# Kernel optimization log

Measured on AMD Instinct MI355X. Metric: run time of the kernel, lower is better.

## Reference

```python
import jax, jax.numpy as jnp
import numpy as np

HEADS = 8
DIM_HEAD = 64
SCALE = DIM_HEAD ** -0.5
QUERY_DIM = 512
CTX_DIM = 64
INNER = HEADS * DIM_HEAD  # 512
GATE_HID = 32


def setup_inputs() -> dict:
    key = jax.random.key(0)
    ks = jax.random.split(key, 11)
    B, N, M = 4, 2048, 2048
    s = lambda fan: 1.0 / np.sqrt(fan)
    return {
        "x": jax.random.normal(ks[0], (B, N, QUERY_DIM), dtype=jnp.float32),
        "context": jax.random.normal(ks[1], (B, M, CTX_DIM), dtype=jnp.float32),
        "Wq": jax.random.normal(ks[2], (QUERY_DIM, INNER), dtype=jnp.float32) * s(QUERY_DIM),
        "Wk": jax.random.normal(ks[3], (CTX_DIM, INNER), dtype=jnp.float32) * s(CTX_DIM),
        "Wv": jax.random.normal(ks[4], (CTX_DIM, INNER), dtype=jnp.float32) * s(CTX_DIM),
        "W1": jax.random.normal(ks[5], (CTX_DIM, GATE_HID), dtype=jnp.float32) * s(CTX_DIM),
        "b1": jnp.zeros((GATE_HID,), dtype=jnp.float32),
        "W2": jax.random.normal(ks[6], (GATE_HID, 1), dtype=jnp.float32) * s(GATE_HID),
        "b2": jnp.zeros((1,), dtype=jnp.float32),
        "Wo": jax.random.normal(ks[7], (INNER, QUERY_DIM), dtype=jnp.float32) * s(INNER),
        "bo": jnp.zeros((QUERY_DIM,), dtype=jnp.float32),
    }


def reference(x, context, Wq, Wk, Wv, W1, b1, W2, b2, Wo, bo):
    B, N, _ = x.shape
    M = context.shape[1]
    # visual reliability gate: sigmoid(relu(ctx @ W1 + b1) @ W2 + b2) -> [B, M, 1]
    gate = jax.nn.sigmoid(jax.nn.relu(context @ W1 + b1) @ W2 + b2)
    ctx = context * gate
    # projections
    q = (x @ Wq).reshape(B, N, HEADS, DIM_HEAD).transpose(0, 2, 1, 3)    # [B,H,N,D]
    k = (ctx @ Wk).reshape(B, M, HEADS, DIM_HEAD).transpose(0, 2, 1, 3)  # [B,H,M,D]
    v = (ctx @ Wv).reshape(B, M, HEADS, DIM_HEAD).transpose(0, 2, 1, 3)  # [B,H,M,D]
    # scaled dot-product attention (full score matrix, as in source)
    sim = jnp.einsum('bhid,bhjd->bhij', q, k) * SCALE
    attn = jax.nn.softmax(sim, axis=-1)
    out = jnp.einsum('bhij,bhjd->bhid', attn, v)
    out = out.transpose(0, 2, 1, 3).reshape(B, N, INNER)
    return out @ Wo + bo
```

## Files before the change

kernel.cpp:

```cpp
#include <hip/hip_runtime.h>

typedef unsigned short u16;
typedef unsigned int u32;
using frag16 = __attribute__((ext_vector_type(8))) short;
using facc   = __attribute__((ext_vector_type(4))) float;
using facc16 = __attribute__((ext_vector_type(16))) float;

#define DEV static __device__ __forceinline__

DEV u16 f2bf(float f) {
  union { float f; unsigned u; } v; v.f = f;
  unsigned r = v.u + 0x7fffu + ((v.u >> 16) & 1u);
  return (u16)(r >> 16);
}
DEV unsigned fbits(float f) {
  union { float f; unsigned u; } v; v.f = f;
  return v.u;
}
DEV unsigned pkbf(float lo, float hi) {
  return __builtin_amdgcn_perm(fbits(hi) + 0x8000u, fbits(lo) + 0x8000u, 0x07060302u);
}
DEV unsigned pkbf_t(float lo, float hi) {
  return __builtin_amdgcn_perm(fbits(hi), fbits(lo), 0x07060302u);
}
DEV void gld16(const u16* g, u16* l) {
  __builtin_amdgcn_global_load_lds(
      (__attribute__((address_space(1))) unsigned int*)(g),
      (__attribute__((address_space(3))) unsigned int*)(l), 16, 0, 0);
}

__global__ __launch_bounds__(256) void prep_gate_kernel(const float4* __restrict__ x,
    const float* __restrict__ Wq, const float* __restrict__ Wk,
    const float* __restrict__ Wv, const float* __restrict__ Wo,
    const float* __restrict__ ctx, const float* __restrict__ W1,
    const float* __restrict__ b1, const float* __restrict__ W2,
    const float* __restrict__ b2,
    u16* __restrict__ xb, u16* __restrict__ WqT, u16* __restrict__ WkT,
    u16* __restrict__ WvT, u16* __restrict__ WoT, u16* __restrict__ gctx) {
  int bid = blockIdx.x;
  if (bid < 4096) {
    int id = bid * 256 + threadIdx.x;
    float4 v = x[id];
    ushort4 o;
    o.x = f2bf(v.x); o.y = f2bf(v.y); o.z = f2bf(v.z); o.w = f2bf(v.w);
    *(ushort4*)(xb + (size_t)id * 4) = o;
  } else if (bid < 4240) {
    int job = bid - 4096;
    const float* W; u16* WT; int K, tile;
    if (job < 64)      { W = Wq; WT = WqT; K = 512; tile = job; }
    else if (job < 72) { W = Wk; WT = WkT; K = 64;  tile = job - 64; }
    else if (job < 80) { W = Wv; WT = WvT; K = 64;  tile = job - 72; }
    else               { W = Wo; WT = WoT; K = 512; tile = job - 80; }
    int tilesK = K >> 6;
    int tr = tile % tilesK, tc = tile / tilesK;
    __shared__ float tl[64][65];
    int c = threadIdx.x & 63, r4 = threadIdx.x >> 6;
    #pragma unroll
    for (int it = 0; it < 16; ++it) {
      int kk = it * 4 + r4;
      tl[kk][c] = W[(size_t)(tr * 64 + kk) * 512 + tc * 64 + c];
    }
    __syncthreads();
    #pragma unroll
    for (int it = 0; it < 16; ++it) {
      int nn = it * 4 + r4;
      WT[(size_t)(tc * 64 + nn) * K + tr * 64 + c] = f2bf(tl[c][nn]);
    }
  } else {
    int wave = threadIdx.x >> 6, lane = threadIdx.x & 63;
    int row = (bid - 4240) * 4 + wave;
    __shared__ float sc[4][64];
    float cv = ctx[(size_t)row * 64 + lane];
    sc[wave][lane] = cv;
    __syncthreads();
    float h = 0.f;
    if (lane < 32) {
      h = b1[lane];
      #pragma unroll
      for (int i = 0; i < 64; ++i) h += sc[wave][i] * W1[i * 32 + lane];
      h = fmaxf(h, 0.f) * W2[lane];
    }
    #pragma unroll
    for (int off = 32; off; off >>= 1) h += __shfl_xor(h, off);
    float g = 1.f / (1.f + __expf(-(h + b2[0])));
    gctx[(size_t)row * 64 + lane] = f2bf(cv * g);
  }
}

template<int MODE>
DEV void gemm128_body(const u16* __restrict__ A, const u16* __restrict__ BT,
                      void* __restrict__ Cp, const float* __restrict__ bias,
                      int m0, int n0, float scale,
                      u16* As0, u16* As1, u16* Bs0, u16* Bs1) {
  const int K = 512, N = 512;
  const int lane = threadIdx.x & 63, wave = threadIdx.x >> 6;
  const int quad = lane >> 4, l16 = lane & 15;
  const int wr = wave >> 1, wc = wave & 1;

  const u16* gA = A + (size_t)(m0 + wave * 32 + (lane >> 2)) * K + (lane & 3) * 8;
  const u16* gB = BT + (size_t)(n0 + wave * 16 + (lane >> 2)) * K + (lane & 3) * 8;

  facc acc[4][2] = {};

  for (int k0 = 0; k0 < K; k0 += 64) {
    if (k0) __syncthreads();
    gld16(gA + k0,           As0 + wave * 1024);
    gld16(gA + 16 * K + k0,  As0 + wave * 1024 + 512);
    gld16(gA + k0 + 32,          As1 + wave * 1024);
    gld16(gA + 16 * K + k0 + 32, As1 + wave * 1024 + 512);
    gld16(gB + k0,      Bs0 + wave * 512);
    gld16(gB + k0 + 32, Bs1 + wave * 512);
    __syncthreads();

    #pragma unroll
    for (int hh = 0; hh < 2; ++hh) {
      const u16* Ah = hh ? As1 : As0;
      const u16* Bh = hh ? Bs1 : Bs0;
      frag16 af[4], bf[2];
      #pragma unroll
      for (int rt = 0; rt < 4; ++rt)
        af[rt] = *(const frag16*)(Ah + (wr * 64 + rt * 16 + l16) * 32 + quad * 8);
      #pragma unroll
      for (int ct = 0; ct < 2; ++ct)
        bf[ct] = *(const frag16*)(Bh + (wc * 32 + ct * 16 + l16) * 32 + quad * 8);
      #pragma unroll
      for (int rt = 0; rt < 4; ++rt)
        #pragma unroll
        for (int ct = 0; ct < 2; ++ct)
          acc[rt][ct] = __builtin_amdgcn_mfma_f32_16x16x32_bf16(af[rt], bf[ct], acc[rt][ct], 0, 0, 0);
    }
  }

  #pragma unroll
  for (int rt = 0; rt < 4; ++rt) {
    #pragma unroll
    for (int ct = 0; ct < 2; ++ct) {
      int col = n0 + wc * 32 + ct * 16 + l16;
      int r0g = m0 + wr * 64 + rt * 16 + quad * 4;
      if (MODE == 0) {
        u16* C = (u16*)Cp;
        #pragma unroll
        for (int r = 0; r < 4; ++r)
          C[(size_t)(r0g + r) * N + col] = f2bf(acc[rt][ct][r] * scale);
      } else {
        float* C = (float*)Cp;
        float bv = bias[col];
        #pragma unroll
        for (int r = 0; r < 4; ++r)
          C[(size_t)(r0g + r) * N + col] = acc[rt][ct][r] + bv;
      }
    }
  }
}

__global__ __launch_bounds__(256) void proj_kernel(const u16* __restrict__ xb,
    const u16* __restrict__ WqT, u16* __restrict__ qb,
    const u16* __restrict__ gctx, const u16* __restrict__ BkT,
    const u16* __restrict__ BvT, u16* __restrict__ Kp, u16* __restrict__ Vp) {
  __shared__ __align__(16) u16 As0[128 * 32], As1[128 * 32];
  __shared__ __align__(16) u16 Bs0[64 * 32], Bs1[64 * 32];
  int bid = blockIdx.x;
  if (bid < 512) {
    int n0 = (bid & 7) * 64, m0 = (bid >> 3) * 128;
    gemm128_body<0>(xb, WqT, qb, nullptr, m0, n0,
                    0.125f * 1.4426950408889634f, As0, As1, Bs0, Bs1);
    return;
  }
  bid -= 512;
  const int Kd = 64;
  int lane = threadIdx.x & 63, wave = threadIdx.x >> 6;
  int quad = lane >> 4, l16 = lane & 15;
  int wr = wave >> 1, wc = wave & 1;
  int rowBase = (bid >> 3) * 64 + wr * 32;
  int colBase = (bid & 7) * 64 + wc * 32;
  facc ak[2][2] = {}, av[2][2] = {};
  const u16* a0 = gctx + (size_t)(rowBase + l16) * Kd + quad * 8;
  const u16* a1 = a0 + (size_t)16 * Kd;
  const u16* bk0 = BkT + (size_t)(colBase + l16) * Kd + quad * 8;
  const u16* bk1 = bk0 + (size_t)16 * Kd;
  const u16* bv0 = BvT + (size_t)(colBase + l16) * Kd + quad * 8;
  const u16* bv1 = bv0 + (size_t)16 * Kd;
  #pragma unroll
  for (int kk = 0; kk < Kd; kk += 32) {
    frag16 af0 = *(const frag16*)(a0 + kk);
    frag16 af1 = *(const frag16*)(a1 + kk);
    frag16 k0 = *(const frag16*)(bk0 + kk);
    frag16 k1 = *(const frag16*)(bk1 + kk);
    frag16 v0 = *(const frag16*)(bv0 + kk);
    frag16 v1 = *(const frag16*)(bv1 + kk);
    ak[0][0] = __builtin_amdgcn_mfma_f32_16x16x32_bf16(af0, k0, ak[0][0], 0, 0, 0);
    ak[0][1] = __builtin_amdgcn_mfma_f32_16x16x32_bf16(af0, k1, ak[0][1], 0, 0, 0);
    ak[1][0] = __builtin_amdgcn_mfma_f32_16x16x32_bf16(af1, k0, ak[1][0], 0, 0, 0);
    ak[1][1] = __builtin_amdgcn_mfma_f32_16x16x32_bf16(af1, k1, ak[1][1], 0, 0, 0);
    av[0][0] = __builtin_amdgcn_mfma_f32_16x16x32_bf16(af0, v0, av[0][0], 0, 0, 0);
    av[0][1] = __builtin_amdgcn_mfma_f32_16x16x32_bf16(af0, v1, av[0][1], 0, 0, 0);
    av[1][0] = __builtin_amdgcn_mfma_f32_16x16x32_bf16(af1, v0, av[1][0], 0, 0, 0);
    av[1][1] = __builtin_amdgcn_mfma_f32_16x16x32_bf16(af1, v1, av[1][1], 0, 0, 0);
  }
  #pragma unroll
  for (int rt = 0; rt < 2; ++rt) {
    #pragma unroll
    for (int ct = 0; ct < 2; ++ct) {
      int col = colBase + ct * 16 + l16;
      int r0g = rowBase + rt * 16 + quad * 4;
      int hh = col >> 6, d = col & 63;
      int b = r0g >> 11;
      #pragma unroll
      for (int r = 0; r < 4; ++r) {
        int m = (r0g + r) & 2047;
        size_t addr = ((((size_t)(b * 8 + hh) * 64 + (m >> 5)) * 4 + (d >> 4)) * 64
                       + ((d >> 3) & 1) * 32 + (m & 31)) * 8 + (d & 7);
        Kp[addr] = f2bf(ak[rt][ct][r]);
      }
      int m = r0g & 2047;
      size_t addr = ((((size_t)(b * 8 + hh) * 64 + (m >> 5)) * 4
                      + ((m >> 4) & 1) * 2 + (d >> 5)) * 64
                     + ((m >> 3) & 1) * 32 + (d & 31)) * 8 + (m & 7);
      ushort4 o;
      o.x = f2bf(av[rt][ct][0]); o.y = f2bf(av[rt][ct][1]);
      o.z = f2bf(av[rt][ct][2]); o.w = f2bf(av[rt][ct][3]);
      *(ushort4*)(Vp + addr) = o;
    }
  }
}

__global__ __launch_bounds__(256, 2) void attn_kernel(
    const u16* __restrict__ qb, const u16* __restrict__ Kp,
    const u16* __restrict__ Vp, u16* __restrict__ ob) {
  const int lane = threadIdx.x & 63, wave = threadIdx.x >> 6;
  const int l32 = lane & 31;
  const int hi = lane >> 5;
  const int bid = blockIdx.x;
  const int bh = bid & 31;
  const int qblk = bid >> 5;
  const int b = bh >> 3, h = bh & 7;
  const int q0 = (qblk * 4 + wave) * 32;
  const int rowg = b * 2048 + q0 + l32;

  __shared__ __align__(16) u16 sK[2][2][2048], sV[2][2][2048];

  const u16* qp = qb + (size_t)rowg * 512 + h * 64 + hi * 8;
  frag16 qf0 = *(const frag16*)(qp);
  frag16 qf1 = *(const frag16*)(qp + 16);
  frag16 qf2 = *(const frag16*)(qp + 32);
  frag16 qf3 = *(const frag16*)(qp + 48);

  frag16 ones;
  #pragma unroll
  for (int i = 0; i < 8; ++i) ones[i] = (short)0x3F80;

  facc16 O0 = {}, O1 = {}, Lacc = {};

  const size_t ts = 2048;
  const u16* kpb = Kp + (size_t)(bh * 64) * ts + wave * 512 + lane * 8;
  const u16* vpb = Vp + (size_t)(bh * 64) * ts + wave * 512 + lane * 8;

  gld16(kpb,      sK[0][0] + wave * 512);
  gld16(kpb + ts, sK[0][1] + wave * 512);
  gld16(vpb,      sV[0][0] + wave * 512);
  gld16(vpb + ts, sV[0][1] + wave * 512);

  for (int g = 0; g < 32; ++g) {
    const int p = g & 1;
    __syncthreads();
    if (g + 1 < 32) {
      const size_t t2 = (size_t)(2 * g + 2) * ts;
      gld16(kpb + t2,      sK[p ^ 1][0] + wave * 512);
      gld16(kpb + t2 + ts, sK[p ^ 1][1] + wave * 512);
      gld16(vpb + t2,      sV[p ^ 1][0] + wave * 512);
      gld16(vpb + t2 + ts, sV[p ^ 1][1] + wave * 512);
    }

    frag16 kfa[4], kfb[4];
    #pragma unroll
    for (int i = 0; i < 4; ++i) {
      kfa[i] = *(const frag16*)(sK[p][0] + i * 512 + lane * 8);
      kfb[i] = *(const frag16*)(sK[p][1] + i * 512 + lane * 8);
    }

    facc16 Sa = {}, Sb = {};
    Sa = __builtin_amdgcn_mfma_f32_32x32x16_bf16(kfa[0], qf0, Sa, 0, 0, 0);
    Sb = __builtin_amdgcn_mfma_f32_32x32x16_bf16(kfb[0], qf0, Sb, 0, 0, 0);
    Sa = __builtin_amdgcn_mfma_f32_32x32x16_bf16(kfa[1], qf1, Sa, 0, 0, 0);
    Sb = __builtin_amdgcn_mfma_f32_32x32x16_bf16(kfb[1], qf1, Sb, 0, 0, 0);
    Sa = __builtin_amdgcn_mfma_f32_32x32x16_bf16(kfa[2], qf2, Sa, 0, 0, 0);
    Sb = __builtin_amdgcn_mfma_f32_32x32x16_bf16(kfb[2], qf2, Sb, 0, 0, 0);
    Sa = __builtin_amdgcn_mfma_f32_32x32x16_bf16(kfa[3], qf3, Sa, 0, 0, 0);
    Sb = __builtin_amdgcn_mfma_f32_32x32x16_bf16(kfb[3], qf3, Sb, 0, 0, 0);

    float ea[16], eb[16];
    #pragma unroll
    for (int r = 0; r < 16; ++r) { ea[r] = __builtin_amdgcn_exp2f(Sa[r]);
                                   eb[r] = __builtin_amdgcn_exp2f(Sb[r]); }

    unsigned pua[2][4], pub[2][4];
    #pragma unroll
    for (int c = 0; c < 2; ++c) {
      {
        const float* ee = ea + c * 8;
        unsigned L0 = pkbf_t(ee[0], ee[1]);
        unsigned L1 = pkbf_t(ee[2], ee[3]);
        unsigned H0 = pkbf_t(ee[4], ee[5]);
        unsigned H1 = pkbf_t(ee[6], ee[7]);
        unsigned Y0 = hi ? L0 : H0;
        unsigned Y1 = hi ? L1 : H1;
        unsigned X0 = (unsigned)__shfl_xor((int)Y0, 32);
        unsigned X1 = (unsigned)__shfl_xor((int)Y1, 32);
        pua[c][0] = hi ? X0 : L0;
        pua[c][1] = hi ? X1 : L1;
        pua[c][2] = hi ? H0 : X0;
        pua[c][3] = hi ? H1 : X1;
      }
      {
        const float* ee = eb + c * 8;
        unsigned L0 = pkbf_t(ee[0], ee[1]);
        unsigned L1 = pkbf_t(ee[2], ee[3]);
        unsigned H0 = pkbf_t(ee[4], ee[5]);
        unsigned H1 = pkbf_t(ee[6], ee[7]);
        unsigned Y0 = hi ? L0 : H0;
        unsigned Y1 = hi ? L1 : H1;
        unsigned X0 = (unsigned)__shfl_xor((int)Y0, 32);
        unsigned X1 = (unsigned)__shfl_xor((int)Y1, 32);
        pub[c][0] = hi ? X0 : L0;
        pub[c][1] = hi ? X1 : L1;
        pub[c][2] = hi ? H0 : X0;
        pub[c][3] = hi ? H1 : X1;
      }
    }
    frag16 Pa0 = *(frag16*)&pua[0][0];
    frag16 Pa1 = *(frag16*)&pua[1][0];
    frag16 Pb0 = *(frag16*)&pub[0][0];
    frag16 Pb1 = *(frag16*)&pub[1][0];

    Lacc = __builtin_amdgcn_mfma_f32_32x32x16_bf16(ones, Pa0, Lacc, 0, 0, 0);
    Lacc = __builtin_amdgcn_mfma_f32_32x32x16_bf16(ones, Pa1, Lacc, 0, 0, 0);
    Lacc = __builtin_amdgcn_mfma_f32_32x32x16_bf16(ones, Pb0, Lacc, 0, 0, 0);
    Lacc = __builtin_amdgcn_mfma_f32_32x32x16_bf16(ones, Pb1, Lacc, 0, 0, 0);

    frag16 vfa[4], vfb[4];
    #pragma unroll
    for (int i = 0; i < 4; ++i) {
      vfa[i] = *(const frag16*)(sV[p][0] + i * 512 + lane * 8);
      vfb[i] = *(const frag16*)(sV[p][1] + i * 512 + lane * 8);
    }

    O0 = __builtin_amdgcn_mfma_f32_32x32x16_bf16(vfa[0], Pa0, O0, 0, 0, 0);
    O1 = __builtin_amdgcn_mfma_f32_32x32x16_bf16(vfa[1], Pa0, O1, 0, 0, 0);
    O0 = __builtin_amdgcn_mfma_f32_32x32x16_bf16(vfa[2], Pa1, O0, 0, 0, 0);
    O1 = __builtin_amdgcn_mfma_f32_32x32x16_bf16(vfa[3], Pa1, O1, 0, 0, 0);
    O0 = __builtin_amdgcn_mfma_f32_32x32x16_bf16(vfb[0], Pb0, O0, 0, 0, 0);
    O1 = __builtin_amdgcn_mfma_f32_32x32x16_bf16(vfb[1], Pb0, O1, 0, 0, 0);
    O0 = __builtin_amdgcn_mfma_f32_32x32x16_bf16(vfb[2], Pb1, O0, 0, 0, 0);
    O1 = __builtin_amdgcn_mfma_f32_32x32x16_bf16(vfb[3], Pb1, O1, 0, 0, 0);
  }

  float rinv = 1.0f / Lacc[0];

  u16* op = ob + (size_t)rowg * 512 + h * 64;
  #pragma unroll
  for (int dt = 0; dt < 2; ++dt) {
    #pragma unroll
    for (int rq = 0; rq < 4; ++rq) {
      float v0, v1, v2, v3;
      if (dt == 0) { v0 = O0[rq*4]; v1 = O0[rq*4+1]; v2 = O0[rq*4+2]; v3 = O0[rq*4+3]; }
      else         { v0 = O1[rq*4]; v1 = O1[rq*4+1]; v2 = O1[rq*4+2]; v3 = O1[rq*4+3]; }
      uint2 pk;
      pk.x = pkbf(v0 * rinv, v1 * rinv);
      pk.y = pkbf(v2 * rinv, v3 * rinv);
      int d0 = dt * 32 + 8 * rq + 4 * hi;
      *(uint2*)(op + d0) = pk;
    }
  }
}

__global__ __launch_bounds__(256) void gemm_out(const u16* __restrict__ A,
    const u16* __restrict__ BT, float* __restrict__ C,
    const float* __restrict__ bias) {
  __shared__ __align__(16) u16 As0[128 * 32], As1[128 * 32];
  __shared__ __align__(16) u16 Bs0[64 * 32], Bs1[64 * 32];
  int n0 = (blockIdx.x & 7) * 64, m0 = (blockIdx.x >> 3) * 128;
  gemm128_body<2>(A, BT, C, bias, m0, n0, 1.f, As0, As1, Bs0, Bs1);
}

extern "C" void kernel_launch(void* const* d_in, const int* in_sizes, int n_in,
                              void* d_out, int out_size, void* d_ws, size_t ws_size,
                              hipStream_t stream) {
  const float* x   = (const float*)d_in[0];
  const float* ctx = (const float*)d_in[1];
  const float* Wq  = (const float*)d_in[2];
  const float* Wk  = (const float*)d_in[3];
  const float* Wv  = (const float*)d_in[4];
  const float* W1  = (const float*)d_in[5];
  const float* b1  = (const float*)d_in[6];
  const float* W2  = (const float*)d_in[7];
  const float* b2  = (const float*)d_in[8];
  const float* Wo  = (const float*)d_in[9];
  const float* bo  = (const float*)d_in[10];
  float* out = (float*)d_out;

  char* ws = (char*)d_ws;
  size_t off = 0;
  auto alloc = [&](size_t bytes) {
    char* p = ws + off;
    off += (bytes + 255) & ~(size_t)255;
    return p;
  };
  u16* xb    = (u16*)alloc(8192ull * 512 * 2);
  u16* qb    = (u16*)alloc(8192ull * 512 * 2);
  u16* Kp    = (u16*)alloc(8192ull * 512 * 2);
  u16* Vp    = (u16*)alloc(8192ull * 512 * 2);
  u16* ob    = (u16*)alloc(8192ull * 512 * 2);
  u16* gctx  = (u16*)alloc(8192ull * 64 * 2);
  u16* WqT   = (u16*)alloc(512ull * 512 * 2);
  u16* WkT   = (u16*)alloc(512ull * 64 * 2);
  u16* WvT   = (u16*)alloc(512ull * 64 * 2);
  u16* WoT   = (u16*)alloc(512ull * 512 * 2);

  prep_gate_kernel<<<6288, 256, 0, stream>>>((const float4*)x, Wq, Wk, Wv, Wo,
                                             ctx, W1, b1, W2, b2,
                                             xb, WqT, WkT, WvT, WoT, gctx);
  proj_kernel<<<1536, 256, 0, stream>>>(xb, WqT, qb, gctx, WkT, WvT, Kp, Vp);
  attn_kernel<<<512, 256, 0, stream>>>(qb, Kp, Vp, ob);
  gemm_out<<<512, 256, 0, stream>>>(ob, WoT, out, bo);
}
```

Measured before the change: 166.9 us.

## Software-pipeline attention loop: overlap QK of next tile with softmax/PV of current

Restructures the attention main loop into a two-stage software pipeline: the QK^T MFMAs for the next K/V tile are issued before the exp/pack/PV work of the current tile, with explicit double-buffer staging and fewer barriers per pair of tiles. It also interleaves the row-sum MFMAs with the PV MFMAs and raises wave priority around MFMA bursts via s_setprio. The aim is to hide exp and shuffle latency behind matrix work, at the cost of more live accumulator registers, which may reduce occupancy.

```diff
diff --git a/kernel.cpp b/kernel.cpp
--- a/kernel.cpp
+++ b/kernel.cpp
@@ -250,48 +250,55 @@
   for (int i = 0; i < 8; ++i) ones[i] = (short)0x3F80;
 
   facc16 O0 = {}, O1 = {}, Lacc = {};
+  facc16 SA0, SA1, SB0, SB1;
 
   const size_t ts = 2048;
   const u16* kpb = Kp + (size_t)(bh * 64) * ts + wave * 512 + lane * 8;
   const u16* vpb = Vp + (size_t)(bh * 64) * ts + wave * 512 + lane * 8;
 
-  gld16(kpb,      sK[0][0] + wave * 512);
-  gld16(kpb + ts, sK[0][1] + wave * 512);
-  gld16(vpb,      sV[0][0] + wave * 512);
-  gld16(vpb + ts, sV[0][1] + wave * 512);
-
-  for (int g = 0; g < 32; ++g) {
-    const int p = g & 1;
-    __syncthreads();
-    if (g + 1 < 32) {
-      const size_t t2 = (size_t)(2 * g + 2) * ts;
-      gld16(kpb + t2,      sK[p ^ 1][0] + wave * 512);
-      gld16(kpb + t2 + ts, sK[p ^ 1][1] + wave * 512);
-      gld16(vpb + t2,      sV[p ^ 1][0] + wave * 512);
-      gld16(vpb + t2 + ts, sV[p ^ 1][1] + wave * 512);
-    }
-
+  u16* k0 = &sK[0][0][0]; u16* v0 = &sV[0][0][0];
+  u16* k1 = &sK[1][0][0]; u16* v1 = &sV[1][0][0];
+
+  auto STAGE = [&](int g, u16* dK, u16* dV) {
+    const size_t t2 = (size_t)(2 * g) * ts;
+    gld16(kpb + t2,      dK + wave * 512);
+    gld16(kpb + t2 + ts, dK + 2048 + wave * 512);
+    gld16(vpb + t2,      dV + wave * 512);
+    gld16(vpb + t2 + ts, dV + 2048 + wave * 512);
+  };
+
+  auto QK = [&](const u16* bK, facc16& S0, facc16& S1) {
     frag16 kfa[4], kfb[4];
     #pragma unroll
     for (int i = 0; i < 4; ++i) {
-      kfa[i] = *(const frag16*)(sK[p][0] + i * 512 + lane * 8);
-      kfb[i] = *(const frag16*)(sK[p][1] + i * 512 + lane * 8);
-    }
-
-    facc16 Sa = {}, Sb = {};
-    Sa = __builtin_amdgcn_mfma_f32_32x32x16_bf16(kfa[0], qf0, Sa, 0, 0, 0);
-    Sb = __builtin_amdgcn_mfma_f32_32x32x16_bf16(kfb[0], qf0, Sb, 0, 0, 0);
-    Sa = __builtin_amdgcn_mfma_f32_32x32x16_bf16(kfa[1], qf1, Sa, 0, 0, 0);
-    Sb = __builtin_amdgcn_mfma_f32_32x32x16_bf16(kfb[1], qf1, Sb, 0, 0, 0);
-    Sa = __builtin_amdgcn_mfma_f32_32x32x16_bf16(kfa[2], qf2, Sa, 0, 0, 0);
-    Sb = __builtin_amdgcn_mfma_f32_32x32x16_bf16(kfb[2], qf2, Sb, 0, 0, 0);
-    Sa = __builtin_amdgcn_mfma_f32_32x32x16_bf16(kfa[3], qf3, Sa, 0, 0, 0);
-    Sb = __builtin_amdgcn_mfma_f32_32x32x16_bf16(kfb[3], qf3, Sb, 0, 0, 0);
-
+      kfa[i] = *(const frag16*)(bK + i * 512 + lane * 8);
+      kfb[i] = *(const frag16*)(bK + 2048 + i * 512 + lane * 8);
+    }
+    facc16 sa = {}, sb = {};
+    __builtin_amdgcn_s_setprio(1);
+    sa = __builtin_amdgcn_mfma_f32_32x32x16_bf16(kfa[0], qf0, sa, 0, 0, 0);
+    sb = __builtin_amdgcn_mfma_f32_32x32x16_bf16(kfb[0], qf0, sb, 0, 0, 0);
+    sa = __builtin_amdgcn_mfma_f32_32x32x16_bf16(kfa[1], qf1, sa, 0, 0, 0);
+    sb = __builtin_amdgcn_mfma_f32_32x32x16_bf16(kfb[1], qf1, sb, 0, 0, 0);
+    sa = __builtin_amdgcn_mfma_f32_32x32x16_bf16(kfa[2], qf2, sa, 0, 0, 0);
+    sb = __builtin_amdgcn_mfma_f32_32x32x16_bf16(kfb[2], qf2, sb, 0, 0, 0);
+    sa = __builtin_amdgcn_mfma_f32_32x32x16_bf16(kfa[3], qf3, sa, 0, 0, 0);
+    sb = __builtin_amdgcn_mfma_f32_32x32x16_bf16(kfb[3], qf3, sb, 0, 0, 0);
+    __builtin_amdgcn_s_setprio(0);
+    S0 = sa; S1 = sb;
+  };
+
+  auto EPPV = [&](const facc16& S0, const facc16& S1, const u16* bV) {
+    frag16 vfa[4], vfb[4];
+    #pragma unroll
+    for (int i = 0; i < 4; ++i) {
+      vfa[i] = *(const frag16*)(bV + i * 512 + lane * 8);
+      vfb[i] = *(const frag16*)(bV + 2048 + i * 512 + lane * 8);
+    }
     float ea[16], eb[16];
     #pragma unroll
-    for (int r = 0; r < 16; ++r) { ea[r] = __builtin_amdgcn_exp2f(Sa[r]);
-                                   eb[r] = __builtin_amdgcn_exp2f(Sb[r]); }
+    for (int r = 0; r < 16; ++r) { ea[r] = __builtin_amdgcn_exp2f(S0[r]);
+                                   eb[r] = __builtin_amdgcn_exp2f(S1[r]); }
 
     unsigned pua[2][4], pub[2][4];
     #pragma unroll
@@ -332,27 +339,43 @@
     frag16 Pb0 = *(frag16*)&pub[0][0];
     frag16 Pb1 = *(frag16*)&pub[1][0];
 
+    __builtin_amdgcn_s_setprio(1);
     Lacc = __builtin_amdgcn_mfma_f32_32x32x16_bf16(ones, Pa0, Lacc, 0, 0, 0);
-    Lacc = __builtin_amdgcn_mfma_f32_32x32x16_bf16(ones, Pa1, Lacc, 0, 0, 0);
-    Lacc = __builtin_amdgcn_mfma_f32_32x32x16_bf16(ones, Pb0, Lacc, 0, 0, 0);
-    Lacc = __builtin_amdgcn_mfma_f32_32x32x16_bf16(ones, Pb1, Lacc, 0, 0, 0);
-
-    frag16 vfa[4], vfb[4];
-    #pragma unroll
-    for (int i = 0; i < 4; ++i) {
-      vfa[i] = *(const frag16*)(sV[p][0] + i * 512 + lane * 8);
-      vfb[i] = *(const frag16*)(sV[p][1] + i * 512 + lane * 8);
-    }
-
     O0 = __builtin_amdgcn_mfma_f32_32x32x16_bf16(vfa[0], Pa0, O0, 0, 0, 0);
     O1 = __builtin_amdgcn_mfma_f32_32x32x16_bf16(vfa[1], Pa0, O1, 0, 0, 0);
+    Lacc = __builtin_amdgcn_mfma_f32_32x32x16_bf16(ones, Pa1, Lacc, 0, 0, 0);
     O0 = __builtin_amdgcn_mfma_f32_32x32x16_bf16(vfa[2], Pa1, O0, 0, 0, 0);
     O1 = __builtin_amdgcn_mfma_f32_32x32x16_bf16(vfa[3], Pa1, O1, 0, 0, 0);
+    Lacc = __builtin_amdgcn_mfma_f32_32x32x16_bf16(ones, Pb0, Lacc, 0, 0, 0);
     O0 = __builtin_amdgcn_mfma_f32_32x32x16_bf16(vfb[0], Pb0, O0, 0, 0, 0);
     O1 = __builtin_amdgcn_mfma_f32_32x32x16_bf16(vfb[1], Pb0, O1, 0, 0, 0);
+    Lacc = __builtin_amdgcn_mfma_f32_32x32x16_bf16(ones, Pb1, Lacc, 0, 0, 0);
     O0 = __builtin_amdgcn_mfma_f32_32x32x16_bf16(vfb[2], Pb1, O0, 0, 0, 0);
     O1 = __builtin_amdgcn_mfma_f32_32x32x16_bf16(vfb[3], Pb1, O1, 0, 0, 0);
-  }
+    __builtin_amdgcn_s_setprio(0);
+  };
+
+  STAGE(0, k0, v0);
+  __syncthreads();
+  STAGE(1, k1, v1);
+  QK(k0, SA0, SA1);
+
+  #pragma unroll 1
+  for (int gg = 0; gg < 15; ++gg) {
+    const int g = 2 * gg;
+    EPPV(SA0, SA1, v0);
+    __syncthreads();
+    STAGE(g + 2, k0, v0);
+    QK(k1, SB0, SB1);
+    EPPV(SB0, SB1, v1);
+    __syncthreads();
+    STAGE(g + 3, k1, v1);
+    QK(k0, SA0, SA1);
+  }
+  EPPV(SA0, SA1, v0);
+  __syncthreads();
+  QK(k1, SB0, SB1);
+  EPPV(SB0, SB1, v1);
 
   float rinv = 1.0f / Lacc[0];
 
@@ -361,12 +384,12 @@
   for (int dt = 0; dt < 2; ++dt) {
     #pragma unroll
     for (int rq = 0; rq < 4; ++rq) {
-      float v0, v1, v2, v3;
-      if (dt == 0) { v0 = O0[rq*4]; v1 = O0[rq*4+1]; v2 = O0[rq*4+2]; v3 = O0[rq*4+3]; }
-      else         { v0 = O1[rq*4]; v1 = O1[rq*4+1]; v2 = O1[rq*4+2]; v3 = O1[rq*4+3]; }
+      float v0e, v1e, v2e, v3e;
+      if (dt == 0) { v0e = O0[rq*4]; v1e = O0[rq*4+1]; v2e = O0[rq*4+2]; v3e = O0[rq*4+3]; }
+      else         { v0e = O1[rq*4]; v1e = O1[rq*4+1]; v2e = O1[rq*4+2]; v3e = O1[rq*4+3]; }
       uint2 pk;
-      pk.x = pkbf(v0 * rinv, v1 * rinv);
-      pk.y = pkbf(v2 * rinv, v3 * rinv);
+      pk.x = pkbf(v0e * rinv, v1e * rinv);
+      pk.y = pkbf(v2e * rinv, v3e * rinv);
       int d0 = dt * 32 + 8 * rq + 4 * hi;
       *(uint2*)(op + d0) = pk;
     }
```

Result: no change. 169.0 us (+1.3%).

## Triple-buffer K/V tiles in attention with explicit vmcnt waits

Applied to the files above, without the earlier changes.

Moves the attention kernel's K/V shared-memory staging from double to triple buffering, prefetching two tiles ahead. Each iteration waits only on the older tile's loads via explicit s_waitcnt vmcnt and a raw barrier, and the next prefetch is issued after the K fragments are read, so it can be a single barrier per iteration. Shared memory rises from 32KB to 48KB per block, which may affect the two-blocks-per-CU occupancy, and correctness now depends on the hand-counted vmcnt value matching the number of outstanding loads.

```diff
diff --git a/kernel.cpp b/kernel.cpp
--- a/kernel.cpp
+++ b/kernel.cpp
@@ -237,7 +237,7 @@
   const int q0 = (qblk * 4 + wave) * 32;
   const int rowg = b * 2048 + q0 + l32;
 
-  __shared__ __align__(16) u16 sK[2][2][2048], sV[2][2][2048];
+  __shared__ __align__(16) u16 sK[3][2][2048], sV[3][2][2048];
 
   const u16* qp = qb + (size_t)rowg * 512 + h * 64 + hi * 8;
   frag16 qf0 = *(const frag16*)(qp);
@@ -255,27 +255,40 @@
   const u16* kpb = Kp + (size_t)(bh * 64) * ts + wave * 512 + lane * 8;
   const u16* vpb = Vp + (size_t)(bh * 64) * ts + wave * 512 + lane * 8;
 
-  gld16(kpb,      sK[0][0] + wave * 512);
-  gld16(kpb + ts, sK[0][1] + wave * 512);
-  gld16(vpb,      sV[0][0] + wave * 512);
-  gld16(vpb + ts, sV[0][1] + wave * 512);
-
+  auto STAGE = [&](int g, int buf) {
+    const size_t t2 = (size_t)(2 * g) * ts;
+    gld16(kpb + t2,      &sK[buf][0][0] + wave * 512);
+    gld16(kpb + t2 + ts, &sK[buf][1][0] + wave * 512);
+    gld16(vpb + t2,      &sV[buf][0][0] + wave * 512);
+    gld16(vpb + t2 + ts, &sV[buf][1][0] + wave * 512);
+  };
+
+  STAGE(0, 0);
+  STAGE(1, 1);
+
+  int p = 0;
+  #pragma unroll 1
   for (int g = 0; g < 32; ++g) {
-    const int p = g & 1;
-    __syncthreads();
-    if (g + 1 < 32) {
-      const size_t t2 = (size_t)(2 * g + 2) * ts;
-      gld16(kpb + t2,      sK[p ^ 1][0] + wave * 512);
-      gld16(kpb + t2 + ts, sK[p ^ 1][1] + wave * 512);
-      gld16(vpb + t2,      sV[p ^ 1][0] + wave * 512);
-      gld16(vpb + t2 + ts, sV[p ^ 1][1] + wave * 512);
-    }
+    if (g < 31) {
+      asm volatile("s_waitcnt vmcnt(4) lgkmcnt(0)" ::: "memory");
+    } else {
+      asm volatile("s_waitcnt vmcnt(0) lgkmcnt(0)" ::: "memory");
+    }
+    __builtin_amdgcn_s_barrier();
+
+    const u16* kbase = &sK[p][0][0];
+    const u16* vbase = &sV[p][0][0];
 
     frag16 kfa[4], kfb[4];
     #pragma unroll
     for (int i = 0; i < 4; ++i) {
-      kfa[i] = *(const frag16*)(sK[p][0] + i * 512 + lane * 8);
-      kfb[i] = *(const frag16*)(sK[p][1] + i * 512 + lane * 8);
+      kfa[i] = *(const frag16*)(kbase + i * 512 + lane * 8);
+      kfb[i] = *(const frag16*)(kbase + 2048 + i * 512 + lane * 8);
+    }
+
+    if (g + 2 < 32) {
+      int ps = p + 2; if (ps >= 3) ps -= 3;
+      STAGE(g + 2, ps);
     }
 
     facc16 Sa = {}, Sb = {};
@@ -340,8 +353,8 @@
     frag16 vfa[4], vfb[4];
     #pragma unroll
     for (int i = 0; i < 4; ++i) {
-      vfa[i] = *(const frag16*)(sV[p][0] + i * 512 + lane * 8);
-      vfb[i] = *(const frag16*)(sV[p][1] + i * 512 + lane * 8);
+      vfa[i] = *(const frag16*)(vbase + i * 512 + lane * 8);
+      vfb[i] = *(const frag16*)(vbase + 2048 + i * 512 + lane * 8);
     }
 
     O0 = __builtin_amdgcn_mfma_f32_32x32x16_bf16(vfa[0], Pa0, O0, 0, 0, 0);
@@ -352,6 +365,8 @@
     O1 = __builtin_amdgcn_mfma_f32_32x32x16_bf16(vfb[1], Pb0, O1, 0, 0, 0);
     O0 = __builtin_amdgcn_mfma_f32_32x32x16_bf16(vfb[2], Pb1, O0, 0, 0, 0);
     O1 = __builtin_amdgcn_mfma_f32_32x32x16_bf16(vfb[3], Pb1, O1, 0, 0, 0);
+
+    ++p; if (p == 3) p = 0;
   }
 
   float rinv = 1.0f / Lacc[0];
@@ -361,12 +376,12 @@
   for (int dt = 0; dt < 2; ++dt) {
     #pragma unroll
     for (int rq = 0; rq < 4; ++rq) {
-      float v0, v1, v2, v3;
-      if (dt == 0) { v0 = O0[rq*4]; v1 = O0[rq*4+1]; v2 = O0[rq*4+2]; v3 = O0[rq*4+3]; }
-      else         { v0 = O1[rq*4]; v1 = O1[rq*4+1]; v2 = O1[rq*4+2]; v3 = O1[rq*4+3]; }
+      float v0e, v1e, v2e, v3e;
+      if (dt == 0) { v0e = O0[rq*4]; v1e = O0[rq*4+1]; v2e = O0[rq*4+2]; v3e = O0[rq*4+3]; }
+      else         { v0e = O1[rq*4]; v1e = O1[rq*4+1]; v2e = O1[rq*4+2]; v3e = O1[rq*4+3]; }
       uint2 pk;
-      pk.x = pkbf(v0 * rinv, v1 * rinv);
-      pk.y = pkbf(v2 * rinv, v3 * rinv);
+      pk.x = pkbf(v0e * rinv, v1e * rinv);
+      pk.y = pkbf(v2e * rinv, v3e * rinv);
       int d0 = dt * 32 + 8 * rq + 4 * hi;
       *(uint2*)(op + d0) = pk;
     }
```

Result: no change. 168.5 us (+0.9%).

## Double-buffer GEMM LDS tiles with XOR swizzle and coarsen prep kernel

Applied to the files above, without the earlier changes.

Rewrites the shared 128x64 GEMM body so the next K-slab is prefetched into a second LDS buffer while the current one feeds the MFMAs, with one barrier per iteration instead of two. The LDS layout becomes 64-wide rows with an XOR chunk swizzle, meant to avoid bank conflicts on fragment reads. The prep kernel converts 16 floats per thread (fewer blocks), and the gate MLP now uses all 64 lanes by splitting the reduction in halves. LDS use per block doubles, which may lower occupancy.

```diff
diff --git a/kernel.cpp b/kernel.cpp
--- a/kernel.cpp
+++ b/kernel.cpp
@@ -38,14 +38,19 @@
     u16* __restrict__ xb, u16* __restrict__ WqT, u16* __restrict__ WkT,
     u16* __restrict__ WvT, u16* __restrict__ WoT, u16* __restrict__ gctx) {
   int bid = blockIdx.x;
-  if (bid < 4096) {
+  if (bid < 1024) {
     int id = bid * 256 + threadIdx.x;
-    float4 v = x[id];
-    ushort4 o;
-    o.x = f2bf(v.x); o.y = f2bf(v.y); o.z = f2bf(v.z); o.w = f2bf(v.w);
-    *(ushort4*)(xb + (size_t)id * 4) = o;
-  } else if (bid < 4240) {
-    int job = bid - 4096;
+    const float4* xp = x + (size_t)id * 4;
+    u16* op = xb + (size_t)id * 16;
+    #pragma unroll
+    for (int j = 0; j < 4; ++j) {
+      float4 v = xp[j];
+      ushort4 o;
+      o.x = f2bf(v.x); o.y = f2bf(v.y); o.z = f2bf(v.z); o.w = f2bf(v.w);
+      *(ushort4*)(op + j * 4) = o;
+    }
+  } else if (bid < 1168) {
+    int job = bid - 1024;
     const float* W; u16* WT; int K, tile;
     if (job < 64)      { W = Wq; WT = WqT; K = 512; tile = job; }
     else if (job < 72) { W = Wk; WT = WkT; K = 64;  tile = job - 64; }
@@ -68,21 +73,23 @@
     }
   } else {
     int wave = threadIdx.x >> 6, lane = threadIdx.x & 63;
-    int row = (bid - 4240) * 4 + wave;
+    int hi = lane >> 5, hl = lane & 31;
+    int row = (bid - 1168) * 4 + wave;
     __shared__ float sc[4][64];
     float cv = ctx[(size_t)row * 64 + lane];
     sc[wave][lane] = cv;
     __syncthreads();
-    float h = 0.f;
-    if (lane < 32) {
-      h = b1[lane];
-      #pragma unroll
-      for (int i = 0; i < 64; ++i) h += sc[wave][i] * W1[i * 32 + lane];
-      h = fmaxf(h, 0.f) * W2[lane];
-    }
-    #pragma unroll
-    for (int off = 32; off; off >>= 1) h += __shfl_xor(h, off);
-    float g = 1.f / (1.f + __expf(-(h + b2[0])));
+    float hp = 0.f;
+    #pragma unroll
+    for (int i = 0; i < 32; ++i) {
+      int ii = hi * 32 + i;
+      hp += sc[wave][ii] * W1[ii * 32 + hl];
+    }
+    hp += __shfl_xor(hp, 32);
+    float hr = fmaxf(hp + b1[hl], 0.f) * W2[hl];
+    #pragma unroll
+    for (int off = 16; off; off >>= 1) hr += __shfl_xor(hr, off);
+    float g = 1.f / (1.f + __expf(-(hr + b2[0])));
     gctx[(size_t)row * 64 + lane] = f2bf(cv * g);
   }
 }
@@ -91,44 +98,59 @@
 DEV void gemm128_body(const u16* __restrict__ A, const u16* __restrict__ BT,
                       void* __restrict__ Cp, const float* __restrict__ bias,
                       int m0, int n0, float scale,
-                      u16* As0, u16* As1, u16* Bs0, u16* Bs1) {
+                      u16* As, u16* Bs) {
   const int K = 512, N = 512;
   const int lane = threadIdx.x & 63, wave = threadIdx.x >> 6;
   const int quad = lane >> 4, l16 = lane & 15;
   const int wr = wave >> 1, wc = wave & 1;
 
-  const u16* gA = A + (size_t)(m0 + wave * 32 + (lane >> 2)) * K + (lane & 3) * 8;
-  const u16* gB = BT + (size_t)(n0 + wave * 16 + (lane >> 2)) * K + (lane & 3) * 8;
+  const int sr  = lane >> 3;
+  const int sc8 = ((lane & 7) ^ sr) * 8;
+  const u16* gA = A + (size_t)(m0 + wave * 32 + sr) * K + sc8;
+  const u16* gB = BT + (size_t)(n0 + wave * 16 + sr) * K + sc8;
+
+  auto STAGE = [&](int k0, int buf) {
+    u16* dA = As + buf * 8192 + wave * 2048;
+    #pragma unroll
+    for (int j = 0; j < 4; ++j)
+      gld16(gA + k0 + (size_t)(j * 8) * K, dA + j * 512);
+    u16* dB = Bs + buf * 4096 + wave * 1024;
+    #pragma unroll
+    for (int j = 0; j < 2; ++j)
+      gld16(gB + k0 + (size_t)(j * 8) * K, dB + j * 512);
+  };
 
   facc acc[4][2] = {};
-
+  STAGE(0, 0);
+  int buf = 0;
   for (int k0 = 0; k0 < K; k0 += 64) {
-    if (k0) __syncthreads();
-    gld16(gA + k0,           As0 + wave * 1024);
-    gld16(gA + 16 * K + k0,  As0 + wave * 1024 + 512);
-    gld16(gA + k0 + 32,          As1 + wave * 1024);
-    gld16(gA + 16 * K + k0 + 32, As1 + wave * 1024 + 512);
-    gld16(gB + k0,      Bs0 + wave * 512);
-    gld16(gB + k0 + 32, Bs1 + wave * 512);
-    __syncthreads();
-
+    asm volatile("s_waitcnt vmcnt(0)" ::: "memory");
+    __builtin_amdgcn_s_barrier();
+    if (k0 + 64 < K) STAGE(k0 + 64, buf ^ 1);
+    const u16* Ah = As + buf * 8192;
+    const u16* Bh = Bs + buf * 4096;
     #pragma unroll
     for (int hh = 0; hh < 2; ++hh) {
-      const u16* Ah = hh ? As1 : As0;
-      const u16* Bh = hh ? Bs1 : Bs0;
-      frag16 af[4], bf[2];
+      frag16 af[4], bfr[2];
       #pragma unroll
-      for (int rt = 0; rt < 4; ++rt)
-        af[rt] = *(const frag16*)(Ah + (wr * 64 + rt * 16 + l16) * 32 + quad * 8);
+      for (int rt = 0; rt < 4; ++rt) {
+        int row = wr * 64 + rt * 16 + l16;
+        int ch = (hh * 4 + quad) ^ (row & 7);
+        af[rt] = *(const frag16*)(Ah + row * 64 + ch * 8);
+      }
       #pragma unroll
-      for (int ct = 0; ct < 2; ++ct)
-        bf[ct] = *(const frag16*)(Bh + (wc * 32 + ct * 16 + l16) * 32 + quad * 8);
+      for (int ct = 0; ct < 2; ++ct) {
+        int row = wc * 32 + ct * 16 + l16;
+        int ch = (hh * 4 + quad) ^ (row & 7);
+        bfr[ct] = *(const frag16*)(Bh + row * 64 + ch * 8);
+      }
       #pragma unroll
       for (int rt = 0; rt < 4; ++rt)
         #pragma unroll
         for (int ct = 0; ct < 2; ++ct)
-          acc[rt][ct] = __builtin_amdgcn_mfma_f32_16x16x32_bf16(af[rt], bf[ct], acc[rt][ct], 0, 0, 0);
-    }
+          acc[rt][ct] = __builtin_amdgcn_mfma_f32_16x16x32_bf16(af[rt], bfr[ct], acc[rt][ct], 0, 0, 0);
+    }
+    buf ^= 1;
   }
 
   #pragma unroll
@@ -157,13 +179,13 @@
     const u16* __restrict__ WqT, u16* __restrict__ qb,
     const u16* __restrict__ gctx, const u16* __restrict__ BkT,
     const u16* __restrict__ BvT, u16* __restrict__ Kp, u16* __restrict__ Vp) {
-  __shared__ __align__(16) u16 As0[128 * 32], As1[128 * 32];
-  __shared__ __align__(16) u16 Bs0[64 * 32], Bs1[64 * 32];
+  __shared__ __align__(16) u16 As[2 * 128 * 64];
+  __shared__ __align__(16) u16 Bs[2 * 64 * 64];
   int bid = blockIdx.x;
   if (bid < 512) {
     int n0 = (bid & 7) * 64, m0 = (bid >> 3) * 128;
     gemm128_body<0>(xb, WqT, qb, nullptr, m0, n0,
-                    0.125f * 1.4426950408889634f, As0, As1, Bs0, Bs1);
+                    0.125f * 1.4426950408889634f, As, Bs);
     return;
   }
   bid -= 512;
@@ -376,10 +398,10 @@
 __global__ __launch_bounds__(256) void gemm_out(const u16* __restrict__ A,
     const u16* __restrict__ BT, float* __restrict__ C,
     const float* __restrict__ bias) {
-  __shared__ __align__(16) u16 As0[128 * 32], As1[128 * 32];
-  __shared__ __align__(16) u16 Bs0[64 * 32], Bs1[64 * 32];
+  __shared__ __align__(16) u16 As[2 * 128 * 64];
+  __shared__ __align__(16) u16 Bs[2 * 64 * 64];
   int n0 = (blockIdx.x & 7) * 64, m0 = (blockIdx.x >> 3) * 128;
-  gemm128_body<2>(A, BT, C, bias, m0, n0, 1.f, As0, As1, Bs0, Bs1);
+  gemm128_body<2>(A, BT, C, bias, m0, n0, 1.f, As, Bs);
 }
 
 extern "C" void kernel_launch(void* const* d_in, const int* in_sizes, int n_in,
@@ -416,7 +438,7 @@
   u16* WvT   = (u16*)alloc(512ull * 64 * 2);
   u16* WoT   = (u16*)alloc(512ull * 512 * 2);
 
-  prep_gate_kernel<<<6288, 256, 0, stream>>>((const float4*)x, Wq, Wk, Wv, Wo,
+  prep_gate_kernel<<<3216, 256, 0, stream>>>((const float4*)x, Wq, Wk, Wv, Wo,
                                              ctx, W1, b1, W2, b2,
                                              xb, WqT, WkT, WvT, WoT, gctx);
   proj_kernel<<<1536, 256, 0, stream>>>(xb, WqT, qb, gctx, WkT, WvT, Kp, Vp);
```

Measured after the change: 167.0 us, median of 2. About the same (+0.1%).
